# Performance work log

Measured on AMD Instinct MI355X. Metric: run time of the kernel, lower is better.

Reference implementation:

```python
import jax, jax.numpy as jnp
import numpy as np

N = 100000
F_IN = 128
HID = 8
HEADS = 8
CLASSES = 40
NEG_SLOPE = 0.2


def gat_conv(x, src, dst, W, a_src, a_dst, bias, heads, out_c):
    # x: [N, F]; W: [F, heads*out_c]; a_src/a_dst: [heads, out_c]; bias: [heads*out_c]
    n = x.shape[0]
    h = (x @ W).reshape(n, heads, out_c)                       # [N, H, C]
    al_src = jnp.sum(h * a_src, axis=-1)                       # [N, H]
    al_dst = jnp.sum(h * a_dst, axis=-1)                       # [N, H]
    e = jax.nn.leaky_relu(al_src[src] + al_dst[dst], NEG_SLOPE)  # [E, H]
    # segment softmax over destination node (PyG softmax over edge_index[1])
    m = jax.ops.segment_max(e, dst, num_segments=n)            # [N, H]
    m = jnp.where(jnp.isfinite(m), m, 0.0)
    ex = jnp.exp(e - m[dst])
    denom = jax.ops.segment_sum(ex, dst, num_segments=n)       # [N, H]
    alpha = ex / denom[dst]                                    # [E, H]
    msg = h[src] * alpha[:, :, None]                           # [E, H, C]
    out = jax.ops.segment_sum(msg, dst, num_segments=n)        # [N, H, C]
    return out.reshape(n, heads * out_c) + bias


def setup_inputs() -> dict:
    key = jax.random.key(0)
    ks = jax.random.split(key, 12)
    E = 1600000
    x = jax.random.normal(ks[0], (N, F_IN), dtype=jnp.float32)
    edge_index = jax.random.randint(ks[1], (2, E), 0, N, dtype=jnp.int32)
    # layer 1: in=F_IN, out=HID, heads=HEADS, concat -> 64 channels
    s1 = 1.0 / np.sqrt(F_IN)
    W1 = jax.random.uniform(ks[2], (F_IN, HEADS * HID), jnp.float32, -s1, s1)
    a_src1 = jax.random.uniform(ks[3], (HEADS, HID), jnp.float32, -0.3, 0.3)
    a_dst1 = jax.random.uniform(ks[4], (HEADS, HID), jnp.float32, -0.3, 0.3)
    b1 = jnp.zeros((HEADS * HID,), jnp.float32)
    # layer 2: in=64, out=CLASSES, heads=1
    d2 = HEADS * HID
    s2 = 1.0 / np.sqrt(d2)
    W2 = jax.random.uniform(ks[5], (d2, CLASSES), jnp.float32, -s2, s2)
    a_src2 = jax.random.uniform(ks[6], (1, CLASSES), jnp.float32, -0.3, 0.3)
    a_dst2 = jax.random.uniform(ks[7], (1, CLASSES), jnp.float32, -0.3, 0.3)
    b2 = jnp.zeros((CLASSES,), jnp.float32)
    return {"x": x, "edge_index": edge_index, "W1": W1, "a_src1": a_src1,
            "a_dst1": a_dst1, "b1": b1, "W2": W2, "a_src2": a_src2,
            "a_dst2": a_dst2, "b2": b2}


def reference(x, edge_index, W1, a_src1, a_dst1, b1, W2, a_src2, a_dst2, b2):
    # PyG GATConv adds self-loops by default
    loops = jnp.arange(N, dtype=edge_index.dtype)
    src = jnp.concatenate([edge_index[0], loops])
    dst = jnp.concatenate([edge_index[1], loops])
    h = gat_conv(x, src, dst, W1, a_src1, a_dst1, b1, HEADS, HID)
    h = jax.nn.relu(h)  # dropout is identity in eval mode
    out = gat_conv(h, src, dst, W2, a_src2, a_dst2, b2, 1, CLASSES)
    return jax.nn.log_softmax(out, axis=1)
```

## Files before the change

kernel.cpp:

```cpp
#include <hip/hip_runtime.h>
#include <hip/hip_bf16.h>
#include <math.h>

#define FIN 128
#define HID 8
#define HEADS 8
#define C1 64
#define CLS 40
#define NSLOPE 0.2f
#define NINF (-__builtin_inff())

typedef __hip_bfloat16 bf16;
typedef unsigned int uint32;
typedef int vint4 __attribute__((ext_vector_type(4)));

__device__ __forceinline__ float lrelu(float x) { return x >= 0.f ? x : NSLOPE * x; }
__device__ __forceinline__ vint4 ldnt4(const int* p) {
    return __builtin_nontemporal_load((const vint4*)p);
}
__device__ __forceinline__ float bfLO(uint32 u) { return __uint_as_float(u << 16); }
__device__ __forceinline__ float bfHI(uint32 u) { return __uint_as_float(u & 0xffff0000u); }

__global__ void k_deg(const int* __restrict__ ei, int E, int* __restrict__ deg) {
    int idx = blockIdx.x * blockDim.x + threadIdx.x;
    int e0 = idx * 4;
    if (e0 + 3 < E) {
        vint4 dv = ldnt4(ei + E + e0);
        atomicAdd(&deg[dv.x], 1); atomicAdd(&deg[dv.y], 1);
        atomicAdd(&deg[dv.z], 1); atomicAdd(&deg[dv.w], 1);
    } else {
        int e_end = min(e0 + 4, E);
        for (int e = e0; e < e_end; ++e) atomicAdd(&deg[ei[E + e]], 1);
    }
}

__global__ __launch_bounds__(256) void k_scan1(const int* __restrict__ deg,
    int* __restrict__ rowstart, int* __restrict__ bsum, int n) {
    __shared__ int sm[256];
    int t = threadIdx.x, i = blockIdx.x * 256 + t;
    int v = (i < n) ? deg[i] + 1 : 0;
    sm[t] = v; __syncthreads();
    int x = v;
    for (int off = 1; off < 256; off <<= 1) {
        int tv = (t >= off) ? sm[t - off] : 0;
        __syncthreads();
        x += tv; sm[t] = x; __syncthreads();
    }
    if (i < n) rowstart[i] = x - v;
    if (t == 255) bsum[blockIdx.x] = x;
}

__global__ __launch_bounds__(512) void k_scan2(int* __restrict__ bsum, int nb) {
    __shared__ int sm[512];
    int t = threadIdx.x;
    int v = (t < nb) ? bsum[t] : 0;
    sm[t] = v; __syncthreads();
    int x = v;
    for (int off = 1; off < 512; off <<= 1) {
        int tv = (t >= off) ? sm[t - off] : 0;
        __syncthreads();
        x += tv; sm[t] = x; __syncthreads();
    }
    if (t < nb) bsum[t] = x - v;
}

__global__ void k_scan3(int* __restrict__ rowstart, const int* __restrict__ bsum,
                        int n, int total) {
    int i = blockIdx.x * blockDim.x + threadIdx.x;
    if (i < n) rowstart[i] += bsum[i >> 8];
    if (i == 0) rowstart[n] = total;
}

__global__ __launch_bounds__(256) void k_scatter(const int* __restrict__ ei,
    int E, int En, int n, int* __restrict__ rowcur, int* __restrict__ csr) {
    int g = blockIdx.x & 7;
    int per8 = (n + 7) >> 3;
    int lo = g * per8, hi = min(n, lo + per8);
    int idx = (blockIdx.x >> 3) * 256 + threadIdx.x;
    int e0 = idx * 4;
    if (e0 + 3 < E) {
        vint4 dv = ldnt4(ei + E + e0);
        vint4 sv = ldnt4(ei + e0);
        if (dv.x >= lo && dv.x < hi) csr[atomicAdd(&rowcur[dv.x], 1)] = sv.x;
        if (dv.y >= lo && dv.y < hi) csr[atomicAdd(&rowcur[dv.y], 1)] = sv.y;
        if (dv.z >= lo && dv.z < hi) csr[atomicAdd(&rowcur[dv.z], 1)] = sv.z;
        if (dv.w >= lo && dv.w < hi) csr[atomicAdd(&rowcur[dv.w], 1)] = sv.w;
    } else {
        int e_end = min(e0 + 4, En);
        for (int e = e0; e < e_end; ++e) {
            int s, d;
            if (e < E) { s = ei[e]; d = ei[E + e]; } else { s = d = e - E; }
            if (d >= lo && d < hi) csr[atomicAdd(&rowcur[d], 1)] = s;
        }
    }
}

__global__ __launch_bounds__(256) void gemm1_kernel(
    const float* __restrict__ x, const float* __restrict__ W1,
    const float* __restrict__ a_src, const float* __restrict__ a_dst,
    bf16* __restrict__ h1b, float* __restrict__ alS, float* __restrict__ alD, int n) {
    __shared__ float4 Wl[FIN][C1 / 4];
    __shared__ float xs[64][FIN + 4];
    int t = threadIdx.x;
    const float4* W4 = (const float4*)W1;
    for (int i = t; i < FIN * (C1 / 4); i += 256) Wl[i / (C1 / 4)][i % (C1 / 4)] = W4[i];
    int node0 = blockIdx.x * 64;
    for (int i = t; i < 64 * (FIN / 4); i += 256) {
        int r = i / (FIN / 4), c = i % (FIN / 4);
        int nn = node0 + r;
        float4 v = {0.f, 0.f, 0.f, 0.f};
        if (nn < n) v = ((const float4*)x)[(size_t)nn * (FIN / 4) + c];
        *(float4*)&xs[r][c * 4] = v;
    }
    __syncthreads();
    int cg = t & 15, ng = t >> 4;
    int head = cg >> 1, hc = (cg & 1) * 4;
    float acc[4][4];
    #pragma unroll
    for (int i = 0; i < 4; ++i)
        for (int j = 0; j < 4; ++j) acc[i][j] = 0.f;
    #pragma unroll 2
    for (int k = 0; k < FIN; ++k) {
        float4 w = Wl[k][cg];
        #pragma unroll
        for (int i = 0; i < 4; ++i) {
            float xv = xs[ng * 4 + i][k];
            acc[i][0] += xv * w.x; acc[i][1] += xv * w.y;
            acc[i][2] += xv * w.z; acc[i][3] += xv * w.w;
        }
    }
    float a_s[4], a_d[4];
    #pragma unroll
    for (int j = 0; j < 4; ++j) {
        a_s[j] = a_src[head * HID + hc + j];
        a_d[j] = a_dst[head * HID + hc + j];
    }
    #pragma unroll
    for (int i = 0; i < 4; ++i) {
        int node = node0 + ng * 4 + i;
        float as = acc[i][0] * a_s[0] + acc[i][1] * a_s[1]
                 + acc[i][2] * a_s[2] + acc[i][3] * a_s[3];
        float ad = acc[i][0] * a_d[0] + acc[i][1] * a_d[1]
                 + acc[i][2] * a_d[2] + acc[i][3] * a_d[3];
        as += __shfl_xor(as, 1, 64);
        ad += __shfl_xor(ad, 1, 64);
        if (node < n) {
            union { ushort4 u; bf16 b[4]; } pk;
            #pragma unroll
            for (int j = 0; j < 4; ++j) pk.b[j] = __float2bfloat16(acc[i][j]);
            ((ushort4*)h1b)[(size_t)node * (C1 / 4) + cg] = pk.u;
            if ((cg & 1) == 0) {
                alS[node * HEADS + head] = as;
                alD[node * HEADS + head] = ad;
            }
        }
    }
}

__global__ __launch_bounds__(256) void k_agg1(
    const int* __restrict__ csr, const int* __restrict__ rowend,
    const int* __restrict__ deg,
    const float* __restrict__ alS, const float* __restrict__ alD,
    const bf16* __restrict__ h1b, const float* __restrict__ b1,
    const float* __restrict__ W2, const float* __restrict__ aS2,
    const float* __restrict__ aD2,
    bf16* __restrict__ h2b, float* __restrict__ alS2, float* __restrict__ alD2,
    int n) {
    __shared__ int    ls[4][64];
    __shared__ float4 lp4[4][128];
    __shared__ float  xrow[4][64];
    __shared__ float  Wl[C1][CLS];
    int t = threadIdx.x;
    for (int i = t; i < C1 * CLS; i += 256) Wl[i / CLS][i % CLS] = W2[i];
    __syncthreads();
    int lane = t & 63, wv = t >> 6;
    int c32 = lane & 31;
    int par = lane >> 5;
    int hp  = c32 >> 2;
    const float* lpf = (const float*)&lp4[wv][0];
    const uint32* h1u = (const uint32*)h1b;
    int stride = gridDim.x * 4;

    for (int d = blockIdx.x * 4 + wv; d < n; d += stride) {
        float4 ad0 = *(const float4*)(alD + d * HEADS);
        float4 ad1 = *(const float4*)(alD + d * HEADS + 4);
        float adh[8] = {ad0.x, ad0.y, ad0.z, ad0.w, ad1.x, ad1.y, ad1.z, ad1.w};
        int cnt  = deg[d] + 1;
        int base = rowend[d] - cnt;
        float accx = 0.f, accy = 0.f, den = 0.f;
        for (int jb = 0; jb < cnt; jb += 64) {
            int ec = min(64, cnt - jb);
            int jj = jb + lane;
            bool on = jj < cnt;
            int s = on ? csr[base + jj] : 0;
            ls[wv][lane] = s;
            float4 a0 = *(const float4*)(alS + s * HEADS);
            float4 a1 = *(const float4*)(alS + s * HEADS + 4);
            float av[8] = {a0.x, a0.y, a0.z, a0.w, a1.x, a1.y, a1.z, a1.w};
            float pv[8];
            #pragma unroll
            for (int h = 0; h < 8; ++h)
                pv[h] = on ? __expf(lrelu(av[h] + adh[h])) : 0.f;
            lp4[wv][lane * 2]     = make_float4(pv[0], pv[1], pv[2], pv[3]);
            lp4[wv][lane * 2 + 1] = make_float4(pv[4], pv[5], pv[6], pv[7]);
            int j = 0;
            for (; j + 8 <= ec; j += 8) {
                int j0 = j + par, j1 = j + 2 + par, j2 = j + 4 + par, j3 = j + 6 + par;
                int s0 = ls[wv][j0], s1 = ls[wv][j1];
                int s2 = ls[wv][j2], s3 = ls[wv][j3];
                float p0 = lpf[j0 * 8 + hp], p1 = lpf[j1 * 8 + hp];
                float p2 = lpf[j2 * 8 + hp], p3 = lpf[j3 * 8 + hp];
                uint32 u0 = h1u[s0 * 32 + c32], u1 = h1u[s1 * 32 + c32];
                uint32 u2 = h1u[s2 * 32 + c32], u3 = h1u[s3 * 32 + c32];
                accx = fmaf(p0, bfLO(u0), accx); accy = fmaf(p0, bfHI(u0), accy);
                accx = fmaf(p1, bfLO(u1), accx); accy = fmaf(p1, bfHI(u1), accy);
                accx = fmaf(p2, bfLO(u2), accx); accy = fmaf(p2, bfHI(u2), accy);
                accx = fmaf(p3, bfLO(u3), accx); accy = fmaf(p3, bfHI(u3), accy);
                den += p0 + p1 + p2 + p3;
            }
            for (; j < ec; j += 2) {
                int j0 = j + par;
                int s0 = ls[wv][j0];
                float p0 = lpf[j0 * 8 + hp];
                uint32 u0 = h1u[s0 * 32 + c32];
                accx = fmaf(p0, bfLO(u0), accx);
                accy = fmaf(p0, bfHI(u0), accy);
                den += p0;
            }
        }
        accx += __shfl_xor(accx, 32, 64);
        accy += __shfl_xor(accy, 32, 64);
        den  += __shfl_xor(den, 32, 64);
        if (lane < 32) {
            float2 bb = *(const float2*)(b1 + 2 * c32);
            float vx = accx / den + bb.x;
            float vy = accy / den + bb.y;
            vx = vx > 0.f ? vx : 0.f;
            vy = vy > 0.f ? vy : 0.f;
            *(float2*)&xrow[wv][2 * c32] = make_float2(vx, vy);
        }
        bool act = lane < CLS;
        float h2c = 0.f;
        if (act) {
            #pragma unroll 8
            for (int k = 0; k < C1; ++k) h2c = fmaf(xrow[wv][k], Wl[k][lane], h2c);
        }
        float as2 = act ? h2c * aS2[lane] : 0.f;
        float ad2 = act ? h2c * aD2[lane] : 0.f;
        #pragma unroll
        for (int off = 1; off < 64; off <<= 1) {
            as2 += __shfl_xor(as2, off, 64);
            ad2 += __shfl_xor(ad2, off, 64);
        }
        if (act) h2b[d * CLS + lane] = __float2bfloat16(h2c);
        if (lane == 0) { alS2[d] = as2; alD2[d] = ad2; }
    }
}

__global__ __launch_bounds__(256) void k_agg2(
    const int* __restrict__ csr, const int* __restrict__ rowend,
    const int* __restrict__ deg,
    const float* __restrict__ alS, const float* __restrict__ alD,
    const bf16* __restrict__ h2b, const float* __restrict__ b2,
    float* __restrict__ out, int n) {
    __shared__ int2 lsp[4][64];
    int lane = threadIdx.x & 63, wv = threadIdx.x >> 6;
    int d = blockIdx.x * 4 + wv;
    if (d >= n) return;
    int c32 = lane & 31;
    int par = lane >> 5;
    bool actB = c32 < (CLS / 2);
    const uint32* h2u = (const uint32*)h2b;
    float ad = alD[d];
    int cnt  = deg[d] + 1;
    int base = rowend[d] - cnt;
    float accx = 0.f, accy = 0.f, den = 0.f;
    for (int jb = 0; jb < cnt; jb += 64) {
        int ec = min(64, cnt - jb);
        int jj = jb + lane;
        bool on = jj < cnt;
        int s = on ? csr[base + jj] : 0;
        float p = on ? __expf(lrelu(alS[s] + ad)) : 0.f;
        den += p;
        lsp[wv][lane] = make_int2(s, __float_as_int(p));
        if (actB) {
            int j = 0;
            for (; j + 8 <= ec; j += 8) {
                int2 e0 = lsp[wv][j + par],     e1 = lsp[wv][j + 2 + par];
                int2 e2 = lsp[wv][j + 4 + par], e3 = lsp[wv][j + 6 + par];
                uint32 u0 = h2u[e0.x * 20 + c32], u1 = h2u[e1.x * 20 + c32];
                uint32 u2 = h2u[e2.x * 20 + c32], u3 = h2u[e3.x * 20 + c32];
                float p0 = __int_as_float(e0.y), p1 = __int_as_float(e1.y);
                float p2 = __int_as_float(e2.y), p3 = __int_as_float(e3.y);
                accx = fmaf(p0, bfLO(u0), accx); accy = fmaf(p0, bfHI(u0), accy);
                accx = fmaf(p1, bfLO(u1), accx); accy = fmaf(p1, bfHI(u1), accy);
                accx = fmaf(p2, bfLO(u2), accx); accy = fmaf(p2, bfHI(u2), accy);
                accx = fmaf(p3, bfLO(u3), accx); accy = fmaf(p3, bfHI(u3), accy);
            }
            for (; j < ec; j += 2) {
                int2 e0 = lsp[wv][j + par];
                uint32 u0 = h2u[e0.x * 20 + c32];
                float p0 = __int_as_float(e0.y);
                accx = fmaf(p0, bfLO(u0), accx);
                accy = fmaf(p0, bfHI(u0), accy);
            }
        }
    }
    #pragma unroll
    for (int off = 1; off < 64; off <<= 1) den += __shfl_xor(den, off, 64);
    accx += __shfl_xor(accx, 32, 64);
    accy += __shfl_xor(accy, 32, 64);
    bool owner = (lane < 32) && actB;
    float vx = 0.f, vy = 0.f;
    if (owner) {
        float2 bb = *(const float2*)(b2 + 2 * c32);
        vx = accx / den + bb.x;
        vy = accy / den + bb.y;
    }
    float mx = owner ? fmaxf(vx, vy) : NINF;
    #pragma unroll
    for (int off = 1; off < 64; off <<= 1) mx = fmaxf(mx, __shfl_xor(mx, off, 64));
    float sum = owner ? (__expf(vx - mx) + __expf(vy - mx)) : 0.f;
    #pragma unroll
    for (int off = 1; off < 64; off <<= 1) sum += __shfl_xor(sum, off, 64);
    float lse = mx + __logf(sum);
    if (owner)
        *(float2*)(out + (size_t)d * CLS + 2 * c32) = make_float2(vx - lse, vy - lse);
}

extern "C" void kernel_launch(void* const* d_in, const int* in_sizes, int n_in,
                              void* d_out, int out_size, void* d_ws, size_t ws_size,
                              hipStream_t stream) {
    const float* x   = (const float*)d_in[0];
    const int*   ei  = (const int*)d_in[1];
    const float* W1  = (const float*)d_in[2];
    const float* aS1 = (const float*)d_in[3];
    const float* aD1 = (const float*)d_in[4];
    const float* b1  = (const float*)d_in[5];
    const float* W2  = (const float*)d_in[6];
    const float* aS2 = (const float*)d_in[7];
    const float* aD2 = (const float*)d_in[8];
    const float* b2  = (const float*)d_in[9];
    float* out = (float*)d_out;

    int n = in_sizes[0] / FIN;
    int E = in_sizes[1] / 2;
    int En = E + n;

    char* wsb = (char*)d_ws;
    bf16*  h1b  = (bf16*)wsb;
    bf16*  h2b  = h1b + (size_t)n * C1;
    float* alS1 = (float*)(h2b + (size_t)n * CLS);
    float* alD1 = alS1 + (size_t)n * HEADS;
    float* alS2 = alD1 + (size_t)n * HEADS;
    float* alD2 = alS2 + n;
    int*   csr  = (int*)(alD2 + n);
    int*   rowstart = csr + En;
    int*   deg  = rowstart + n + 1;
    int*   bsum = deg + n;

    const int T = 256;
    int nb = (n + 255) / 256;

    (void)hipMemsetAsync(deg, 0, (size_t)n * sizeof(int), stream);
    k_deg<<<(E / 4 + T - 1) / T, T, 0, stream>>>(ei, E, deg);
    k_scan1<<<nb, T, 0, stream>>>(deg, rowstart, bsum, n);
    k_scan2<<<1, 512, 0, stream>>>(bsum, nb);
    k_scan3<<<nb, T, 0, stream>>>(rowstart, bsum, n, En);
    int chunks = (En + 1023) / 1024;
    k_scatter<<<chunks * 8, T, 0, stream>>>(ei, E, En, n, rowstart, csr);

    gemm1_kernel<<<(n + 63) / 64, T, 0, stream>>>(x, W1, aS1, aD1, h1b, alS1, alD1, n);
    k_agg1<<<2048, T, 0, stream>>>(csr, rowstart, deg, alS1, alD1, h1b, b1,
                                   W2, aS2, aD2, h2b, alS2, alD2, n);

    k_agg2<<<(n + 3) / 4, T, 0, stream>>>(csr, rowstart, deg, alS2, alD2, h2b, b2, out, n);
}
```

Measured before the change: 344.3 us.

## Widen gather loads to 8-byte bf16 quads and process four edges per wave step

Both aggregation kernels now have each lane load 4 bf16 channels (8 bytes) per gathered row instead of 2, so a wave covers four edges per step with 16-lane groups rather than two edges with 32-lane groups. Layer 1 stores its attention probabilities transposed per head in shared memory with padding, reuses the index buffer as the row scratch, and unrolls 16 edges per iteration. The intent is fewer gather instructions and more memory-level parallelism per wave on the irregular neighbour loads. In exchange it adds more cross-lane shuffle reductions, and in layer 2 six of every sixteen lanes sit idle.

```diff
diff --git a/kernel.cpp b/kernel.cpp
--- a/kernel.cpp
+++ b/kernel.cpp
@@ -13,6 +13,7 @@
 typedef __hip_bfloat16 bf16;
 typedef unsigned int uint32;
 typedef int vint4 __attribute__((ext_vector_type(4)));
+typedef unsigned int vuint2 __attribute__((ext_vector_type(2)));
 
 __device__ __forceinline__ float lrelu(float x) { return x >= 0.f ? x : NSLOPE * x; }
 __device__ __forceinline__ vint4 ldnt4(const int* p) {
@@ -166,84 +167,72 @@
     const float* __restrict__ aD2,
     bf16* __restrict__ h2b, float* __restrict__ alS2, float* __restrict__ alD2,
     int n) {
-    __shared__ int    ls[4][64];
-    __shared__ float4 lp4[4][128];
-    __shared__ float  xrow[4][64];
-    __shared__ float  Wl[C1][CLS];
+    __shared__ int   ls[4][64];
+    __shared__ float lpT[4][8][66];
+    __shared__ float Wl[C1][CLS];
     int t = threadIdx.x;
     for (int i = t; i < C1 * CLS; i += 256) Wl[i / CLS][i % CLS] = W2[i];
     __syncthreads();
     int lane = t & 63, wv = t >> 6;
-    int c32 = lane & 31;
-    int par = lane >> 5;
-    int hp  = c32 >> 2;
-    const float* lpf = (const float*)&lp4[wv][0];
-    const uint32* h1u = (const uint32*)h1b;
+    int c16 = lane & 15;
+    int q   = lane >> 4;
+    int hq  = c16 >> 1;
+    const vuint2* h1u2 = (const vuint2*)h1b;
+    float* xrow = (float*)ls[wv];
     int stride = gridDim.x * 4;
 
     for (int d = blockIdx.x * 4 + wv; d < n; d += stride) {
-        float4 ad0 = *(const float4*)(alD + d * HEADS);
-        float4 ad1 = *(const float4*)(alD + d * HEADS + 4);
+        float4 ad0 = *(const float4*)(alD + (size_t)d * HEADS);
+        float4 ad1 = *(const float4*)(alD + (size_t)d * HEADS + 4);
         float adh[8] = {ad0.x, ad0.y, ad0.z, ad0.w, ad1.x, ad1.y, ad1.z, ad1.w};
         int cnt  = deg[d] + 1;
         int base = rowend[d] - cnt;
-        float accx = 0.f, accy = 0.f, den = 0.f;
+        float a0 = 0.f, a1 = 0.f, a2 = 0.f, a3 = 0.f, den = 0.f;
         for (int jb = 0; jb < cnt; jb += 64) {
             int ec = min(64, cnt - jb);
             int jj = jb + lane;
             bool on = jj < cnt;
             int s = on ? csr[base + jj] : 0;
             ls[wv][lane] = s;
-            float4 a0 = *(const float4*)(alS + s * HEADS);
-            float4 a1 = *(const float4*)(alS + s * HEADS + 4);
-            float av[8] = {a0.x, a0.y, a0.z, a0.w, a1.x, a1.y, a1.z, a1.w};
-            float pv[8];
+            float4 s0v = *(const float4*)(alS + (size_t)s * HEADS);
+            float4 s1v = *(const float4*)(alS + (size_t)s * HEADS + 4);
+            float av[8] = {s0v.x, s0v.y, s0v.z, s0v.w, s1v.x, s1v.y, s1v.z, s1v.w};
             #pragma unroll
             for (int h = 0; h < 8; ++h)
-                pv[h] = on ? __expf(lrelu(av[h] + adh[h])) : 0.f;
-            lp4[wv][lane * 2]     = make_float4(pv[0], pv[1], pv[2], pv[3]);
-            lp4[wv][lane * 2 + 1] = make_float4(pv[4], pv[5], pv[6], pv[7]);
+                lpT[wv][h][lane] = on ? __expf(lrelu(av[h] + adh[h])) : 0.f;
+            #define STEP1(J) {                                              \
+                int e_ = (J) + q;                                           \
+                int s_ = ls[wv][e_];                                        \
+                float p_ = lpT[wv][hq][e_];                                 \
+                vuint2 u_ = h1u2[(size_t)s_ * 16 + c16];                    \
+                a0 = fmaf(p_, bfLO(u_.x), a0); a1 = fmaf(p_, bfHI(u_.x), a1);\
+                a2 = fmaf(p_, bfLO(u_.y), a2); a3 = fmaf(p_, bfHI(u_.y), a3);\
+                den += p_; }
             int j = 0;
-            for (; j + 8 <= ec; j += 8) {
-                int j0 = j + par, j1 = j + 2 + par, j2 = j + 4 + par, j3 = j + 6 + par;
-                int s0 = ls[wv][j0], s1 = ls[wv][j1];
-                int s2 = ls[wv][j2], s3 = ls[wv][j3];
-                float p0 = lpf[j0 * 8 + hp], p1 = lpf[j1 * 8 + hp];
-                float p2 = lpf[j2 * 8 + hp], p3 = lpf[j3 * 8 + hp];
-                uint32 u0 = h1u[s0 * 32 + c32], u1 = h1u[s1 * 32 + c32];
-                uint32 u2 = h1u[s2 * 32 + c32], u3 = h1u[s3 * 32 + c32];
-                accx = fmaf(p0, bfLO(u0), accx); accy = fmaf(p0, bfHI(u0), accy);
-                accx = fmaf(p1, bfLO(u1), accx); accy = fmaf(p1, bfHI(u1), accy);
-                accx = fmaf(p2, bfLO(u2), accx); accy = fmaf(p2, bfHI(u2), accy);
-                accx = fmaf(p3, bfLO(u3), accx); accy = fmaf(p3, bfHI(u3), accy);
-                den += p0 + p1 + p2 + p3;
+            for (; j + 16 <= ec; j += 16) {
+                STEP1(j) STEP1(j + 4) STEP1(j + 8) STEP1(j + 12)
             }
-            for (; j < ec; j += 2) {
-                int j0 = j + par;
-                int s0 = ls[wv][j0];
-                float p0 = lpf[j0 * 8 + hp];
-                uint32 u0 = h1u[s0 * 32 + c32];
-                accx = fmaf(p0, bfLO(u0), accx);
-                accy = fmaf(p0, bfHI(u0), accy);
-                den += p0;
-            }
-        }
-        accx += __shfl_xor(accx, 32, 64);
-        accy += __shfl_xor(accy, 32, 64);
-        den  += __shfl_xor(den, 32, 64);
-        if (lane < 32) {
-            float2 bb = *(const float2*)(b1 + 2 * c32);
-            float vx = accx / den + bb.x;
-            float vy = accy / den + bb.y;
-            vx = vx > 0.f ? vx : 0.f;
-            vy = vy > 0.f ? vy : 0.f;
-            *(float2*)&xrow[wv][2 * c32] = make_float2(vx, vy);
+            for (; j < ec; j += 4) STEP1(j)
+            #undef STEP1
+        }
+        a0 += __shfl_xor(a0, 16, 64); a0 += __shfl_xor(a0, 32, 64);
+        a1 += __shfl_xor(a1, 16, 64); a1 += __shfl_xor(a1, 32, 64);
+        a2 += __shfl_xor(a2, 16, 64); a2 += __shfl_xor(a2, 32, 64);
+        a3 += __shfl_xor(a3, 16, 64); a3 += __shfl_xor(a3, 32, 64);
+        den += __shfl_xor(den, 16, 64); den += __shfl_xor(den, 32, 64);
+        if (lane < 16) {
+            float4 bb = *(const float4*)(b1 + 4 * c16);
+            float v0 = a0 / den + bb.x, v1 = a1 / den + bb.y;
+            float v2 = a2 / den + bb.z, v3 = a3 / den + bb.w;
+            v0 = v0 > 0.f ? v0 : 0.f; v1 = v1 > 0.f ? v1 : 0.f;
+            v2 = v2 > 0.f ? v2 : 0.f; v3 = v3 > 0.f ? v3 : 0.f;
+            *(float4*)&xrow[4 * c16] = make_float4(v0, v1, v2, v3);
         }
         bool act = lane < CLS;
         float h2c = 0.f;
         if (act) {
             #pragma unroll 8
-            for (int k = 0; k < C1; ++k) h2c = fmaf(xrow[wv][k], Wl[k][lane], h2c);
+            for (int k = 0; k < C1; ++k) h2c = fmaf(xrow[k], Wl[k][lane], h2c);
         }
         float as2 = act ? h2c * aS2[lane] : 0.f;
         float ad2 = act ? h2c * aD2[lane] : 0.f;
@@ -252,7 +241,7 @@
             as2 += __shfl_xor(as2, off, 64);
             ad2 += __shfl_xor(ad2, off, 64);
         }
-        if (act) h2b[d * CLS + lane] = __float2bfloat16(h2c);
+        if (act) h2b[(size_t)d * CLS + lane] = __float2bfloat16(h2c);
         if (lane == 0) { alS2[d] = as2; alD2[d] = ad2; }
     }
 }
@@ -267,14 +256,14 @@
     int lane = threadIdx.x & 63, wv = threadIdx.x >> 6;
     int d = blockIdx.x * 4 + wv;
     if (d >= n) return;
-    int c32 = lane & 31;
-    int par = lane >> 5;
-    bool actB = c32 < (CLS / 2);
-    const uint32* h2u = (const uint32*)h2b;
+    int c16 = lane & 15;
+    int q   = lane >> 4;
+    bool actB = c16 < (CLS / 4);
+    const vuint2* h2u2 = (const vuint2*)h2b;
     float ad = alD[d];
     int cnt  = deg[d] + 1;
     int base = rowend[d] - cnt;
-    float accx = 0.f, accy = 0.f, den = 0.f;
+    float a0 = 0.f, a1 = 0.f, a2 = 0.f, a3 = 0.f, den = 0.f;
     for (int jb = 0; jb < cnt; jb += 64) {
         int ec = min(64, cnt - jb);
         int jj = jb + lane;
@@ -284,48 +273,44 @@
         den += p;
         lsp[wv][lane] = make_int2(s, __float_as_int(p));
         if (actB) {
+            #define STEP2(J) {                                              \
+                int2 e_ = lsp[wv][(J) + q];                                 \
+                float p_ = __int_as_float(e_.y);                            \
+                vuint2 u_ = h2u2[(size_t)e_.x * 10 + c16];                  \
+                a0 = fmaf(p_, bfLO(u_.x), a0); a1 = fmaf(p_, bfHI(u_.x), a1);\
+                a2 = fmaf(p_, bfLO(u_.y), a2); a3 = fmaf(p_, bfHI(u_.y), a3);}
             int j = 0;
-            for (; j + 8 <= ec; j += 8) {
-                int2 e0 = lsp[wv][j + par],     e1 = lsp[wv][j + 2 + par];
-                int2 e2 = lsp[wv][j + 4 + par], e3 = lsp[wv][j + 6 + par];
-                uint32 u0 = h2u[e0.x * 20 + c32], u1 = h2u[e1.x * 20 + c32];
-                uint32 u2 = h2u[e2.x * 20 + c32], u3 = h2u[e3.x * 20 + c32];
-                float p0 = __int_as_float(e0.y), p1 = __int_as_float(e1.y);
-                float p2 = __int_as_float(e2.y), p3 = __int_as_float(e3.y);
-                accx = fmaf(p0, bfLO(u0), accx); accy = fmaf(p0, bfHI(u0), accy);
-                accx = fmaf(p1, bfLO(u1), accx); accy = fmaf(p1, bfHI(u1), accy);
-                accx = fmaf(p2, bfLO(u2), accx); accy = fmaf(p2, bfHI(u2), accy);
-                accx = fmaf(p3, bfLO(u3), accx); accy = fmaf(p3, bfHI(u3), accy);
+            for (; j + 16 <= ec; j += 16) {
+                STEP2(j) STEP2(j + 4) STEP2(j + 8) STEP2(j + 12)
             }
-            for (; j < ec; j += 2) {
-                int2 e0 = lsp[wv][j + par];
-                uint32 u0 = h2u[e0.x * 20 + c32];
-                float p0 = __int_as_float(e0.y);
-                accx = fmaf(p0, bfLO(u0), accx);
-                accy = fmaf(p0, bfHI(u0), accy);
-            }
+            for (; j < ec; j += 4) STEP2(j)
+            #undef STEP2
         }
     }
     #pragma unroll
     for (int off = 1; off < 64; off <<= 1) den += __shfl_xor(den, off, 64);
-    accx += __shfl_xor(accx, 32, 64);
-    accy += __shfl_xor(accy, 32, 64);
-    bool owner = (lane < 32) && actB;
-    float vx = 0.f, vy = 0.f;
+    a0 += __shfl_xor(a0, 16, 64); a0 += __shfl_xor(a0, 32, 64);
+    a1 += __shfl_xor(a1, 16, 64); a1 += __shfl_xor(a1, 32, 64);
+    a2 += __shfl_xor(a2, 16, 64); a2 += __shfl_xor(a2, 32, 64);
+    a3 += __shfl_xor(a3, 16, 64); a3 += __shfl_xor(a3, 32, 64);
+    bool owner = (lane < 16) && actB;
+    float v0 = 0.f, v1 = 0.f, v2 = 0.f, v3 = 0.f;
     if (owner) {
-        float2 bb = *(const float2*)(b2 + 2 * c32);
-        vx = accx / den + bb.x;
-        vy = accy / den + bb.y;
-    }
-    float mx = owner ? fmaxf(vx, vy) : NINF;
+        float4 bb = *(const float4*)(b2 + 4 * c16);
+        v0 = a0 / den + bb.x; v1 = a1 / den + bb.y;
+        v2 = a2 / den + bb.z; v3 = a3 / den + bb.w;
+    }
+    float mx = owner ? fmaxf(fmaxf(v0, v1), fmaxf(v2, v3)) : NINF;
     #pragma unroll
     for (int off = 1; off < 64; off <<= 1) mx = fmaxf(mx, __shfl_xor(mx, off, 64));
-    float sum = owner ? (__expf(vx - mx) + __expf(vy - mx)) : 0.f;
+    float sum = owner ? (__expf(v0 - mx) + __expf(v1 - mx)
+                       + __expf(v2 - mx) + __expf(v3 - mx)) : 0.f;
     #pragma unroll
     for (int off = 1; off < 64; off <<= 1) sum += __shfl_xor(sum, off, 64);
     float lse = mx + __logf(sum);
     if (owner)
-        *(float2*)(out + (size_t)d * CLS + 2 * c32) = make_float2(vx - lse, vy - lse);
+        *(float4*)(out + (size_t)d * CLS + 4 * c16) =
+            make_float4(v0 - lse, v1 - lse, v2 - lse, v3 - lse);
 }
 
 extern "C" void kernel_launch(void* const* d_in, const int* in_sizes, int n_in,
```

Result: slower. 384.1 us (+11.6%).
